# Optimization experiments

Measured on AMD Instinct MI355X. Metric: run time of the kernel, lower is better.

## Reference

```python
import jax, jax.numpy as jnp
import numpy as np


def _fro(x):
    # torch.norm(x, 2) on a matrix flattens -> Frobenius norm
    return jnp.sqrt(jnp.sum(x * x))


def _torch_median(x):
    # torch.median returns the lower of the two middle values for even counts
    f = jnp.sort(x.reshape(-1))
    return f[(f.shape[0] - 1) // 2]


def setup_inputs() -> dict:
    key = jax.random.key(0)
    ks = jax.random.split(key, 6)
    return {
        "c2": jax.random.normal(ks[0], (100, 128, 56, 56), dtype=jnp.float32),
        "c3": jax.random.normal(ks[1], (100, 256, 28, 28), dtype=jnp.float32),
        "vmask1": jax.random.normal(ks[2], (100, 128), dtype=jnp.float32),
        "vmask2": jax.random.normal(ks[3], (100, 256), dtype=jnp.float32),
        "amask1": jax.random.normal(ks[4], (100, 128), dtype=jnp.float32),
        "amask2": jax.random.normal(ks[5], (100, 256), dtype=jnp.float32),
    }


def reference(c2, c3, vmask1, vmask2, amask1, amask2):
    # Vectorized equivalent of the 100x128 / 100x256 scalar-copy loops
    tm1 = c2[:, :, 7, 7]  # [100, 128]
    tm2 = c3[:, :, 3, 3]  # [100, 256]

    p = (_fro(tm1 - vmask1) + _fro(tm2 - vmask2)) / (12800.0 + 25600.0)

    c2m = _torch_median(tm1)
    c3m = _torch_median(tm2)
    b1 = jnp.where(tm1 < c2m, 0.0, 1.0).astype(tm1.dtype)
    b2 = jnp.where(tm2 < c3m, 0.0, 1.0).astype(tm2.dtype)

    q = (_fro(b1 - amask1) + _fro(b2 - amask2)) / (128.0 + 256.0)

    return jnp.stack([p, q])  # [2]: (p, q)
```

## Files before the change

kernel.cpp:

```cpp
#include <hip/hip_runtime.h>
#include <math.h>


#define N1 12800
#define N2 25600
#define K1 6399
#define K2 12799
#define NBINS 4096
#define HSHIFT 20
#define CAP 4096

__device__ __forceinline__ unsigned fkey(float f) {
    unsigned u = __float_as_uint(f);
    return (u & 0x80000000u) ? ~u : (u | 0x80000000u);
}
__device__ __forceinline__ float fkey_inv(unsigned u) {
    return (u & 0x80000000u) ? __uint_as_float(u & 0x7FFFFFFFu)
                             : __uint_as_float(~u);
}

__device__ __forceinline__ float block_reduce(float v, float* red) {
    const int lane = threadIdx.x & 63;
    const int wid  = threadIdx.x >> 6;
    const int nw   = (blockDim.x + 63) >> 6;
#pragma unroll
    for (int o = 32; o > 0; o >>= 1) v += __shfl_down(v, o, 64);
    if (lane == 0) red[wid] = v;
    __syncthreads();
    if (wid == 0) {
        v = (lane < nw) ? red[lane] : 0.f;
#pragma unroll
        for (int o = 8; o > 0; o >>= 1) v += __shfl_down(v, o, 64);
    }
    __syncthreads();
    return v;
}

__global__ __launch_bounds__(256) void gather_kernel(
    const float* __restrict__ c2, const float* __restrict__ c3,
    const float* __restrict__ vm1, const float* __restrict__ vm2,
    float* __restrict__ W1, float* __restrict__ W2,
    float* __restrict__ partial,
    unsigned* __restrict__ hist1, unsigned* __restrict__ hist2)
{
    __shared__ float red[16];
    int g = blockIdx.x * 256 + threadIdx.x;
    float d;
    if (g < N1) {
        float v = c2[(size_t)g * 3136 + 399];
        W1[g] = v;
        d = v - vm1[g];
        atomicAdd(&hist1[fkey(v) >> HSHIFT], 1u);
    } else {
        int j = g - N1;
        float v = c3[(size_t)j * 784 + 87];
        W2[j] = v;
        d = v - vm2[j];
        atomicAdd(&hist2[fkey(v) >> HSHIFT], 1u);
    }
    float ss = block_reduce(d * d, red);
    if (threadIdx.x == 0) partial[blockIdx.x] = ss;
}

__shared__ unsigned sh_h[NBINS];
__shared__ unsigned sh_csum[1024];
__shared__ unsigned sh_wsum[16];
__shared__ unsigned sh_cand[CAP];
__shared__ unsigned sh_bin;
__shared__ int sh_kk, sh_m;
__shared__ unsigned sh_res;

__device__ float hist_select(const float* __restrict__ W, int n, int k,
                             const unsigned* __restrict__ histg)
{
    const int t = threadIdx.x;
    __syncthreads();
    for (int i = t; i < NBINS; i += 1024) sh_h[i] = histg[i];
    __syncthreads();
    unsigned c = sh_h[4*t] + sh_h[4*t+1] + sh_h[4*t+2] + sh_h[4*t+3];
    sh_csum[t] = c;
    unsigned wv = c;
#pragma unroll
    for (int o = 32; o > 0; o >>= 1) wv += __shfl_down(wv, o, 64);
    if ((t & 63) == 0) sh_wsum[t >> 6] = wv;
    __syncthreads();
    if (t == 0) {
        int rem = k;
        int w = 0;
        for (; w < 16; ++w) { unsigned s = sh_wsum[w]; if ((unsigned)rem < s) break; rem -= (int)s; }
        int tc = w * 64;
        for (; tc < (w + 1) * 64; ++tc) { unsigned s = sh_csum[tc]; if ((unsigned)rem < s) break; rem -= (int)s; }
        int b = tc * 4;
        for (; b < tc * 4 + 4; ++b) { unsigned s = sh_h[b]; if ((unsigned)rem < s) break; rem -= (int)s; }
        sh_bin = (unsigned)b;
        sh_kk  = rem;
        sh_m   = 0;
    }
    __syncthreads();
    const unsigned bin = sh_bin;
    for (int i = t; i < n; i += 1024) {
        unsigned u = fkey(W[i]);
        if ((u >> HSHIFT) == bin) {
            int p = atomicAdd(&sh_m, 1);
            if (p < CAP) sh_cand[p] = u;
        }
    }
    __syncthreads();
    const int m  = (sh_m < CAP) ? sh_m : CAP;
    const int kk = sh_kk;
    for (int i = t; i < m; i += 1024) {
        unsigned ui = sh_cand[i];
        int r = 0;
        for (int j = 0; j < m; ++j) {
            unsigned uj = sh_cand[j];
            r += (uj < ui) || (uj == ui && j < i);
        }
        if (r == kk) sh_res = ui;
    }
    __syncthreads();
    float res = fkey_inv(sh_res);
    __syncthreads();
    return res;
}

__global__ __launch_bounds__(1024) void finish_kernel(
    const float* __restrict__ W1, const float* __restrict__ W2,
    const float* __restrict__ partial,
    const unsigned* __restrict__ hist1, const unsigned* __restrict__ hist2,
    const float* __restrict__ am1, const float* __restrict__ am2,
    float* __restrict__ out)
{
    __shared__ float red[16];
    const int t = threadIdx.x;

    float a = (t < 50) ? partial[t] : 0.f;
    float b = (t >= 50 && t < 150) ? partial[t] : 0.f;
    float s1 = block_reduce(a, red);
    float s2 = block_reduce(b, red);

    float m1 = hist_select(W1, N1, K1, hist1);
    float m2 = hist_select(W2, N2, K2, hist2);

    float acc1 = 0.f;
    for (int i = t; i < N1; i += 1024) {
        float bb = (W1[i] < m1) ? 0.f : 1.f;
        float dd = bb - am1[i];
        acc1 += dd * dd;
    }
    float acc2 = 0.f;
    for (int i = t; i < N2; i += 1024) {
        float bb = (W2[i] < m2) ? 0.f : 1.f;
        float dd = bb - am2[i];
        acc2 += dd * dd;
    }
    float t1 = block_reduce(acc1, red);
    float t2 = block_reduce(acc2, red);

    if (t == 0) {
        out[0] = (sqrtf(s1) + sqrtf(s2)) / 38400.f;
        out[1] = (sqrtf(t1) + sqrtf(t2)) / 384.f;
    }
}

extern "C" void kernel_launch(void* const* d_in, const int* in_sizes, int n_in,
                              void* d_out, int out_size, void* d_ws, size_t ws_size,
                              hipStream_t stream) {
    const float* c2  = (const float*)d_in[0];
    const float* c3  = (const float*)d_in[1];
    const float* vm1 = (const float*)d_in[2];
    const float* vm2 = (const float*)d_in[3];
    const float* am1 = (const float*)d_in[4];
    const float* am2 = (const float*)d_in[5];
    float* out = (float*)d_out;

    float* ws = (float*)d_ws;
    float* W1      = ws;
    float* W2      = ws + N1;
    float* partial = ws + N1 + N2;
    unsigned* hist1 = (unsigned*)(ws + 38560);
    unsigned* hist2 = hist1 + NBINS;

    hipMemsetAsync(hist1, 0, 2 * NBINS * sizeof(unsigned), stream);
    gather_kernel<<<150, 256, 0, stream>>>(c2, c3, vm1, vm2, W1, W2, partial,
                                           hist1, hist2);
    finish_kernel<<<1, 1024, 0, stream>>>(W1, W2, partial, hist1, hist2,
                                          am1, am2, out);
}
```

Before: 290.7 us.

## Fold amask loss into histogram bins to skip full binarize pass

The gather kernel now also accumulates, per histogram bin, the sum of (1-2a), along with the sum of a^2, using float atomics. The finish kernel then computes the binarized-mask loss algebraically: it adds a suffix sum over bins above the median bin plus a correction over the candidates in the median bin. This removes the final full pass over W and amask inside the single-block kernel. In exchange it adds float atomics in the gather kernel, makes the float summation order nondeterministic, and lowers the candidate buffer cap to 1024.

```diff
diff --git a/kernel.cpp b/kernel.cpp
--- a/kernel.cpp
+++ b/kernel.cpp
@@ -8,15 +8,11 @@
 #define K2 12799
 #define NBINS 4096
 #define HSHIFT 20
-#define CAP 4096
+#define CAP 1024
 
 __device__ __forceinline__ unsigned fkey(float f) {
     unsigned u = __float_as_uint(f);
     return (u & 0x80000000u) ? ~u : (u | 0x80000000u);
-}
-__device__ __forceinline__ float fkey_inv(unsigned u) {
-    return (u & 0x80000000u) ? __uint_as_float(u & 0x7FFFFFFFu)
-                             : __uint_as_float(~u);
 }
 
 __device__ __forceinline__ float block_reduce(float v, float* red) {
@@ -39,39 +35,44 @@
 __global__ __launch_bounds__(256) void gather_kernel(
     const float* __restrict__ c2, const float* __restrict__ c3,
     const float* __restrict__ vm1, const float* __restrict__ vm2,
+    const float* __restrict__ am1, const float* __restrict__ am2,
     float* __restrict__ W1, float* __restrict__ W2,
-    float* __restrict__ partial,
-    unsigned* __restrict__ hist1, unsigned* __restrict__ hist2)
+    float* __restrict__ partialP, float* __restrict__ partialA2,
+    unsigned* __restrict__ hist1, unsigned* __restrict__ hist2,
+    float* __restrict__ T1, float* __restrict__ T2)
 {
     __shared__ float red[16];
     int g = blockIdx.x * 256 + threadIdx.x;
-    float d;
+    float d, a;
     if (g < N1) {
         float v = c2[(size_t)g * 3136 + 399];
         W1[g] = v;
         d = v - vm1[g];
-        atomicAdd(&hist1[fkey(v) >> HSHIFT], 1u);
+        a = am1[g];
+        unsigned b = fkey(v) >> HSHIFT;
+        atomicAdd(&hist1[b], 1u);
+        atomicAdd(&T1[b], 1.f - 2.f * a);
     } else {
         int j = g - N1;
         float v = c3[(size_t)j * 784 + 87];
         W2[j] = v;
         d = v - vm2[j];
-        atomicAdd(&hist2[fkey(v) >> HSHIFT], 1u);
-    }
-    float ss = block_reduce(d * d, red);
-    if (threadIdx.x == 0) partial[blockIdx.x] = ss;
-}
-
-__shared__ unsigned sh_h[NBINS];
-__shared__ unsigned sh_csum[1024];
-__shared__ unsigned sh_wsum[16];
-__shared__ unsigned sh_cand[CAP];
-__shared__ unsigned sh_bin;
-__shared__ int sh_kk, sh_m;
-__shared__ unsigned sh_res;
-
-__device__ float hist_select(const float* __restrict__ W, int n, int k,
-                             const unsigned* __restrict__ histg)
+        a = am2[j];
+        unsigned b = fkey(v) >> HSHIFT;
+        atomicAdd(&hist2[b], 1u);
+        atomicAdd(&T2[b], 1.f - 2.f * a);
+    }
+    float pss = block_reduce(d * d, red);
+    float ass = block_reduce(a * a, red);
+    if (threadIdx.x == 0) {
+        partialP[blockIdx.x]  = pss;
+        partialA2[blockIdx.x] = ass;
+    }
+}
+
+__device__ void hist_scan(const unsigned* __restrict__ histg, int k,
+                          unsigned* sh_h, unsigned* sh_csum, unsigned* sh_wsum,
+                          int* sh_bin, int* sh_kk)
 {
     const int t = threadIdx.x;
     __syncthreads();
@@ -92,73 +93,96 @@
         for (; tc < (w + 1) * 64; ++tc) { unsigned s = sh_csum[tc]; if ((unsigned)rem < s) break; rem -= (int)s; }
         int b = tc * 4;
         for (; b < tc * 4 + 4; ++b) { unsigned s = sh_h[b]; if ((unsigned)rem < s) break; rem -= (int)s; }
-        sh_bin = (unsigned)b;
-        sh_kk  = rem;
-        sh_m   = 0;
-    }
-    __syncthreads();
-    const unsigned bin = sh_bin;
+        *sh_bin = b;
+        *sh_kk  = rem;
+    }
+    __syncthreads();
+}
+
+__device__ void cand_select(const float* __restrict__ W, int n,
+                            const float* __restrict__ am,
+                            int bin, int kk,
+                            unsigned* cand_u, float* cand_a,
+                            int* sh_m, unsigned* sh_res, float* red,
+                            float* corr)
+{
+    const int t = threadIdx.x;
+    if (t == 0) *sh_m = 0;
+    __syncthreads();
     for (int i = t; i < n; i += 1024) {
         unsigned u = fkey(W[i]);
-        if ((u >> HSHIFT) == bin) {
-            int p = atomicAdd(&sh_m, 1);
-            if (p < CAP) sh_cand[p] = u;
+        if ((int)(u >> HSHIFT) == bin) {
+            int p = atomicAdd(sh_m, 1);
+            if (p < CAP) { cand_u[p] = u; cand_a[p] = am[i]; }
         }
     }
     __syncthreads();
-    const int m  = (sh_m < CAP) ? sh_m : CAP;
-    const int kk = sh_kk;
+    const int m = (*sh_m < CAP) ? *sh_m : CAP;
     for (int i = t; i < m; i += 1024) {
-        unsigned ui = sh_cand[i];
+        unsigned ui = cand_u[i];
         int r = 0;
         for (int j = 0; j < m; ++j) {
-            unsigned uj = sh_cand[j];
+            unsigned uj = cand_u[j];
             r += (uj < ui) || (uj == ui && j < i);
         }
-        if (r == kk) sh_res = ui;
-    }
-    __syncthreads();
-    float res = fkey_inv(sh_res);
-    __syncthreads();
-    return res;
+        if (r == kk) *sh_res = ui;
+    }
+    __syncthreads();
+    const unsigned um = *sh_res;
+    float cc = 0.f;
+    for (int i = t; i < m; i += 1024)
+        if (cand_u[i] >= um) cc += 1.f - 2.f * cand_a[i];
+    float tot = block_reduce(cc, red);
+    if (t == 0) *corr = tot;
+    __syncthreads();
 }
 
 __global__ __launch_bounds__(1024) void finish_kernel(
     const float* __restrict__ W1, const float* __restrict__ W2,
-    const float* __restrict__ partial,
+    const float* __restrict__ partialP, const float* __restrict__ partialA2,
     const unsigned* __restrict__ hist1, const unsigned* __restrict__ hist2,
+    const float* __restrict__ T1, const float* __restrict__ T2,
     const float* __restrict__ am1, const float* __restrict__ am2,
     float* __restrict__ out)
 {
-    __shared__ float red[16];
+    __shared__ unsigned sh_h[NBINS];
+    __shared__ unsigned sh_csum[1024];
+    __shared__ unsigned sh_wsum[16];
+    __shared__ unsigned cand_u[CAP];
+    __shared__ float    cand_a[CAP];
+    __shared__ float    red[16];
+    __shared__ int sh_bin, sh_kk, sh_m;
+    __shared__ unsigned sh_res;
+    __shared__ float sh_corr1, sh_corr2;
+
     const int t = threadIdx.x;
 
-    float a = (t < 50) ? partial[t] : 0.f;
-    float b = (t >= 50 && t < 150) ? partial[t] : 0.f;
-    float s1 = block_reduce(a, red);
-    float s2 = block_reduce(b, red);
-
-    float m1 = hist_select(W1, N1, K1, hist1);
-    float m2 = hist_select(W2, N2, K2, hist2);
-
-    float acc1 = 0.f;
-    for (int i = t; i < N1; i += 1024) {
-        float bb = (W1[i] < m1) ? 0.f : 1.f;
-        float dd = bb - am1[i];
-        acc1 += dd * dd;
-    }
-    float acc2 = 0.f;
-    for (int i = t; i < N2; i += 1024) {
-        float bb = (W2[i] < m2) ? 0.f : 1.f;
-        float dd = bb - am2[i];
-        acc2 += dd * dd;
-    }
-    float t1 = block_reduce(acc1, red);
-    float t2 = block_reduce(acc2, red);
+    float s1  = block_reduce((t < 50) ? partialP[t] : 0.f, red);
+    float s2  = block_reduce((t >= 50 && t < 150) ? partialP[t] : 0.f, red);
+    float a21 = block_reduce((t < 50) ? partialA2[t] : 0.f, red);
+    float a22 = block_reduce((t >= 50 && t < 150) ? partialA2[t] : 0.f, red);
+
+    hist_scan(hist1, K1, sh_h, sh_csum, sh_wsum, &sh_bin, &sh_kk);
+    int b1 = sh_bin, kk1 = sh_kk;
+    float sv = 0.f;
+#pragma unroll
+    for (int j = 0; j < 4; ++j) { int b = 4*t + j; if (b > b1) sv += T1[b]; }
+    float suff1 = block_reduce(sv, red);
+    cand_select(W1, N1, am1, b1, kk1, cand_u, cand_a, &sh_m, &sh_res, red, &sh_corr1);
+
+    hist_scan(hist2, K2, sh_h, sh_csum, sh_wsum, &sh_bin, &sh_kk);
+    int b2 = sh_bin, kk2 = sh_kk;
+    sv = 0.f;
+#pragma unroll
+    for (int j = 0; j < 4; ++j) { int b = 4*t + j; if (b > b2) sv += T2[b]; }
+    float suff2 = block_reduce(sv, red);
+    cand_select(W2, N2, am2, b2, kk2, cand_u, cand_a, &sh_m, &sh_res, red, &sh_corr2);
 
     if (t == 0) {
+        float q1 = a21 + suff1 + sh_corr1;
+        float q2 = a22 + suff2 + sh_corr2;
         out[0] = (sqrtf(s1) + sqrtf(s2)) / 38400.f;
-        out[1] = (sqrtf(t1) + sqrtf(t2)) / 384.f;
+        out[1] = (sqrtf(q1) + sqrtf(q2)) / 384.f;
     }
 }
 
@@ -174,15 +198,19 @@
     float* out = (float*)d_out;
 
     float* ws = (float*)d_ws;
-    float* W1      = ws;
-    float* W2      = ws + N1;
-    float* partial = ws + N1 + N2;
-    unsigned* hist1 = (unsigned*)(ws + 38560);
-    unsigned* hist2 = hist1 + NBINS;
-
-    hipMemsetAsync(hist1, 0, 2 * NBINS * sizeof(unsigned), stream);
-    gather_kernel<<<150, 256, 0, stream>>>(c2, c3, vm1, vm2, W1, W2, partial,
-                                           hist1, hist2);
-    finish_kernel<<<1, 1024, 0, stream>>>(W1, W2, partial, hist1, hist2,
-                                          am1, am2, out);
-}
+    float* W1        = ws;
+    float* W2        = ws + N1;
+    float* partialP  = ws + 38400;
+    float* partialA2 = ws + 38560;
+    unsigned* hist1  = (unsigned*)(ws + 38720);
+    unsigned* hist2  = hist1 + NBINS;
+    float* T1        = (float*)(hist2 + NBINS);
+    float* T2        = T1 + NBINS;
+
+    hipMemsetAsync(hist1, 0, 4 * NBINS * sizeof(unsigned), stream);
+    gather_kernel<<<150, 256, 0, stream>>>(c2, c3, vm1, vm2, am1, am2,
+                                           W1, W2, partialP, partialA2,
+                                           hist1, hist2, T1, T2);
+    finish_kernel<<<1, 1024, 0, stream>>>(W1, W2, partialP, partialA2,
+                                          hist1, hist2, T1, T2, am1, am2, out);
+}
```

Measured after the change: 284.4 us. 1.02x faster.
